# Kernel optimization log

Measured on AMD Instinct MI355X. Metric: run time of the kernel, lower is better.

## Reference

```python
import jax, jax.numpy as jnp
import numpy as np

B, T, F, U = 64, 256, 64, 512  # batch, bid_sequence, features, lstm units


def setup_inputs() -> dict:
    key = jax.random.key(0)
    ks = jax.random.split(key, 8)
    sc = 0.05
    return {
        "inputs": jax.random.normal(ks[0], (B, T, F), jnp.float32),
        "kernel": jax.random.normal(ks[1], (F, 4 * U), jnp.float32) * sc,      # LSTM input kernel (i,f,c,o)
        "rec_kernel": jax.random.normal(ks[2], (U, 4 * U), jnp.float32) * sc,  # LSTM recurrent kernel
        "bias": jax.random.normal(ks[3], (4 * U,), jnp.float32) * sc,          # LSTM bias
        "att_W": jax.random.normal(ks[4], (T, T), jnp.float32) * sc,           # row t = weights of attention_denses[t] (first t cols used)
        "att_b": jax.random.normal(ks[5], (T,), jnp.float32) * sc,             # bias of attention_denses[t]
        "out_W": jax.random.normal(ks[6], (U,), jnp.float32) * sc,             # final Dense(1) kernel
        "out_b": jax.random.normal(ks[7], (), jnp.float32) * sc,               # final Dense(1) bias
    }


def reference(inputs, kernel, rec_kernel, bias, att_W, att_b, out_W, out_b):
    Bs, Ts, _ = inputs.shape
    Us = rec_kernel.shape[0]

    # ---- LSTM (keras LSTMCell, gate order i,f,c,o; sigmoid/tanh) ----
    xz = jnp.einsum('btf,fg->btg', inputs, kernel) + bias  # precompute input projection

    def step(carry, z):
        h, c = carry
        g = z + h @ rec_kernel
        i, f, gc, o = jnp.split(g, 4, axis=-1)
        c = jax.nn.sigmoid(f) * c + jax.nn.sigmoid(i) * jnp.tanh(gc)
        h = jax.nn.sigmoid(o) * jnp.tanh(c)
        return (h, c), h

    init = (jnp.zeros((Bs, Us), inputs.dtype), jnp.zeros((Bs, Us), inputs.dtype))
    _, hs = jax.lax.scan(step, init, jnp.swapaxes(xz, 0, 1))
    x = jnp.swapaxes(hs, 0, 1)  # (B, T, U)

    # ---- attention_loop ----
    # keras Attention([x[:t], [x[t]]]) softmaxes over a single key -> weights are
    # exactly 1, so attn output is x[t] tiled t times; transpose + Dense_t(1)
    # collapses to sum(att_W[t, :t]) * x[t] + att_b[t]. Step 0 passes x[0] through.
    t_idx = jnp.arange(Ts)
    tri = (t_idx[None, :] < t_idx[:, None]).astype(x.dtype)  # row t: first t cols valid
    coef = jnp.where(t_idx == 0, jnp.asarray(1.0, x.dtype), jnp.sum(att_W * tri, axis=1))
    shift = jnp.where(t_idx == 0, jnp.asarray(0.0, x.dtype), att_b)
    att = x * coef[None, :, None] + shift[None, :, None]  # (B, T, U)

    # ---- final Dense(1) + reshape + sigmoid ----
    return jax.nn.sigmoid(jnp.einsum('btu,u->bt', att, out_W) + out_b)  # (B, T)
```

## Files before the change

### kernel.cpp

```cpp
#include <hip/hip_runtime.h>
#include <hip/hip_bf16.h>
#include <string.h>

#define B_ 64
#define T_ 256
#define F_ 64
#define U_ 512
#define G4_ 2048
#define KTOT 576
#define KSTEPS 18

typedef __attribute__((ext_vector_type(8))) short short8;
typedef __attribute__((ext_vector_type(4))) float v4f;
typedef __attribute__((ext_vector_type(4))) int i4;
typedef unsigned short u16;

__device__ __forceinline__ float bf2f(u16 b) {
    unsigned int x = ((unsigned int)b) << 16;
    float f; memcpy(&f, &x, 4); return f;
}
__device__ __forceinline__ u16 f2bf(float f) {
    __hip_bfloat16 h = __float2bfloat16(f);
    u16 b; memcpy(&b, &h, 2); return b;
}
__device__ __forceinline__ float sigmoidf_(float x) { return 1.f / (1.f + __expf(-x)); }
__device__ __forceinline__ float tanhf_(float x) {
    float xc = fminf(15.f, fmaxf(-15.f, x));
    float e = __expf(2.f * xc);
    return (e - 1.f) / (e + 1.f);
}

__device__ __forceinline__ float ldany(const void* p, size_t i, int fg) {
    return fg ? ((const float*)p)[i] : bf2f(((const u16*)p)[i]);
}

#define WS_FLAG   0
#define WS_XB     64
#define WS_WP     2097216
#define WS_H2     4456512
#define WS_DOT    4718656
#define WS_BIASF  4784192
#define WS_ATTWF  4792384
#define WS_ATTBF  5054528
#define WS_OUTWF  5055552
#define WS_OUTBF  5057600
#define WS_NEED   5057920

__global__ __launch_bounds__(256) void detect(const unsigned int* __restrict__ w,
                                              int* __restrict__ flag) {
    __shared__ int votes;
    if (threadIdx.x == 0) votes = 0;
    __syncthreads();
    unsigned int v = w[threadIdx.x];
    int e = (v >> 7) & 0xFF;
    if (e >= 100 && e <= 135) atomicAdd(&votes, 1);
    __syncthreads();
    if (threadIdx.x == 0) *flag = (votes < 200) ? 1 : 0;
}

__global__ __launch_bounds__(256) void convert(const void* __restrict__ x,
                                               const void* __restrict__ bias,
                                               const void* __restrict__ attW,
                                               const void* __restrict__ attb,
                                               const void* __restrict__ outW,
                                               const void* __restrict__ outb,
                                               const int* __restrict__ flag,
                                               u16* __restrict__ xb,
                                               float* __restrict__ biasf,
                                               float* __restrict__ attWf,
                                               float* __restrict__ attbf,
                                               float* __restrict__ outWf,
                                               float* __restrict__ outbf,
                                               float* __restrict__ dot,
                                               unsigned int* __restrict__ h2z) {
    int fg = *flag;
    size_t i = (size_t)blockIdx.x * 256 + threadIdx.x;
    if (i < 1048576) {
        float v = ldany(x, i, fg);
        int b = (int)(i >> 14), t = (int)((i >> 6) & 255), f = (int)(i & 63);
        xb[((size_t)t * B_ + b) * F_ + f] = f2bf(v);
        return;
    }
    i -= 1048576;
    if (i < 2048)  { biasf[i] = ldany(bias, i, fg); return; }
    i -= 2048;
    if (i < 65536) { attWf[i] = ldany(attW, i, fg); return; }
    i -= 65536;
    if (i < 256)   { attbf[i] = ldany(attb, i, fg); return; }
    i -= 256;
    if (i < 512)   { outWf[i] = ldany(outW, i, fg); return; }
    i -= 512;
    if (i < 1)     { outbf[i] = ldany(outb, i, fg); return; }
    i -= 1;
    if (i < 16384) { dot[i] = 0.f; return; }
    i -= 16384;
    if (i < 32768) { h2z[i] = 0u; return; }
}

__global__ __launch_bounds__(256) void pack_w(const void* __restrict__ kin,
                                              const void* __restrict__ krec,
                                              const int* __restrict__ flag,
                                              u16* __restrict__ Wp) {
    int fg = *flag;
    int gid = blockIdx.x * 256 + threadIdx.x;
    int lane = gid & 63;
    int frag = gid >> 6;
    int nt = frag / KSTEPS;
    int ks = frag - nt * KSTEPS;
    int kbase = ks * 32 + (lane >> 4) * 8;
    int cp = nt * 16 + (lane & 15);
    int u = cp >> 2, gate = cp & 3;
    int C = gate * U_ + u;
    short8 v;
    for (int j = 0; j < 8; j++) {
        int k = kbase + j;
        float w = (k < F_) ? ldany(kin, (size_t)k * G4_ + C, fg)
                           : ldany(krec, (size_t)(k - F_) * G4_ + C, fg);
        v[j] = (short)f2bf(w);
    }
    *reinterpret_cast<short8*>(Wp + (size_t)gid * 8) = v;
}

__global__ __launch_bounds__(512, 1) void lstm_persist(const u16* __restrict__ xb,
                                                       const float* __restrict__ biasf,
                                                       const float* __restrict__ outWf,
                                                       const u16* __restrict__ Wp,
                                                       u16* __restrict__ h2,
                                                       float* __restrict__ dot) {
    __shared__ __align__(16) u16 stage[16 * 520];
    __shared__ float dp[32][16][9];

    int tid = threadIdx.x;
    int bid = blockIdx.x;
    int rg = bid & 3;
    int gu = bid >> 2;
    int w = tid >> 6, l = tid & 63;
    int nt = gu * 8 + w;

    short8 W[KSTEPS];
    #pragma unroll
    for (int ks = 0; ks < KSTEPS; ks++)
        W[ks] = *reinterpret_cast<const short8*>(Wp + ((size_t)(nt * KSTEPS + ks) * 64 + l) * 8);

    int arow = rg * 16 + (l & 15);
    int koff = (l >> 4) * 8;
    int plr = 2 * w + (l >> 5);
    int pcol = (l & 31) * 16;
    int e = l & 3;
    int erow = 4 * (l >> 4) + e;
    int unit = 4 * nt + ((l >> 2) & 3);
    int cp = nt * 16 + (l & 15);
    float bc = biasf[(cp & 3) * U_ + (cp >> 2)];
    float wout = outWf[unit];
    float c = 0.f;

    for (int t = 0; t < T_; t++) {
        u16* hcur = h2 + (size_t)(t & 1) * (B_ * U_);
        const u16* hprev = h2 + (size_t)((t + 1) & 1) * (B_ * U_);
        unsigned int wtag = ((unsigned)(t >> 1) & 1u) ^ 1u;
        unsigned int rpat = ((((unsigned)(t - 1) >> 1) & 1u) ^ 1u) * 0x00010001u;

        const u16* xrow = xb + ((size_t)t * B_ + arow) * F_;
        short8 a0 = *reinterpret_cast<const short8*>(xrow + koff);
        short8 a1 = *reinterpret_cast<const short8*>(xrow + 32 + koff);
        v4f accA = {bc, bc, bc, bc};
        v4f accB = {0.f, 0.f, 0.f, 0.f};
        v4f accC = {0.f, 0.f, 0.f, 0.f};
        v4f accD = {0.f, 0.f, 0.f, 0.f};
        accA = __builtin_amdgcn_mfma_f32_16x16x32_bf16(a0, W[0], accA, 0, 0, 0);
        accB = __builtin_amdgcn_mfma_f32_16x16x32_bf16(a1, W[1], accB, 0, 0, 0);
        __builtin_amdgcn_sched_barrier(0);

        i4 q0, q1;
        {
            const void* bp = (const void*)(hprev + (size_t)(rg * 16 + plr) * U_ + pcol);
            int spins = 0;
            for (;;) {
                asm volatile(
                    "global_load_dwordx4 %0, %2, off sc0 sc1\n\t"
                    "global_load_dwordx4 %1, %2, off offset:16 sc0 sc1\n\t"
                    "s_waitcnt vmcnt(0)"
                    : "=v"(q0), "=v"(q1) : "v"(bp) : "memory");
                if (t == 0) break;
                unsigned bad = 0;
                bad |= (((unsigned)q0[0]) ^ rpat) & 0x00010001u;
                bad |= (((unsigned)q0[1]) ^ rpat) & 0x00010001u;
                bad |= (((unsigned)q0[2]) ^ rpat) & 0x00010001u;
                bad |= (((unsigned)q0[3]) ^ rpat) & 0x00010001u;
                bad |= (((unsigned)q1[0]) ^ rpat) & 0x00010001u;
                bad |= (((unsigned)q1[1]) ^ rpat) & 0x00010001u;
                bad |= (((unsigned)q1[2]) ^ rpat) & 0x00010001u;
                bad |= (((unsigned)q1[3]) ^ rpat) & 0x00010001u;
                if (__ballot(bad == 0) == ~0ull) break;
                if (++spins > (1 << 14)) break;
                if (spins > 16)     __builtin_amdgcn_s_sleep(2);
                else if (spins > 3) __builtin_amdgcn_s_sleep(1);
            }
        }
        *reinterpret_cast<i4*>(&stage[plr * 520 + pcol])     = q0;
        *reinterpret_cast<i4*>(&stage[plr * 520 + pcol + 8]) = q1;
        __syncthreads();

        #pragma unroll
        for (int m = 2; m < KSTEPS; m += 4) {
            const u16* srow = &stage[(l & 15) * 520 + koff];
            short8 h0 = *reinterpret_cast<const short8*>(srow + (m - 2) * 32);
            short8 h1 = *reinterpret_cast<const short8*>(srow + (m - 1) * 32);
            short8 h2v = *reinterpret_cast<const short8*>(srow + (m    ) * 32);
            short8 h3 = *reinterpret_cast<const short8*>(srow + (m + 1) * 32);
            accC = __builtin_amdgcn_mfma_f32_16x16x32_bf16(h0, W[m],     accC, 0, 0, 0);
            accD = __builtin_amdgcn_mfma_f32_16x16x32_bf16(h1, W[m + 1], accD, 0, 0, 0);
            accA = __builtin_amdgcn_mfma_f32_16x16x32_bf16(h2v, W[m + 2], accA, 0, 0, 0);
            accB = __builtin_amdgcn_mfma_f32_16x16x32_bf16(h3, W[m + 3], accB, 0, 0, 0);
        }
        v4f acc = (accA + accC) + (accB + accD);

        float g0 = acc[0], g1 = acc[1], g2 = acc[2], g3 = acc[3];
        {
            float t0 = __shfl_xor(g1, 1, 64);
            float t1 = __shfl_xor(g0, 1, 64);
            float t2 = __shfl_xor(g3, 1, 64);
            float t3 = __shfl_xor(g2, 1, 64);
            float b0 = ((0 ^ e) & 1) ? t0 : g0;
            float b1 = ((1 ^ e) & 1) ? t1 : g1;
            float b2 = ((2 ^ e) & 1) ? t2 : g2;
            float b3 = ((3 ^ e) & 1) ? t3 : g3;
            float u0 = __shfl_xor(b2, 2, 64);
            float u1 = __shfl_xor(b3, 2, 64);
            float u2 = __shfl_xor(b0, 2, 64);
            float u3 = __shfl_xor(b1, 2, 64);
            g0 = ((0 ^ e) & 2) ? u0 : b0;
            g1 = ((1 ^ e) & 2) ? u1 : b1;
            g2 = ((2 ^ e) & 2) ? u2 : b2;
            g3 = ((3 ^ e) & 2) ? u3 : b3;
        }

        {
            float ig = sigmoidf_(g0);
            float fg = sigmoidf_(g1);
            float gc = tanhf_(g2);
            float og = sigmoidf_(g3);
            c = fg * c + ig * gc;
            float h = og * tanhf_(c);

            float hp = __shfl_xor(h, 4, 64);
            if (((l >> 2) & 1) == 0) {
                unsigned int pk = (unsigned int)(((unsigned)f2bf(h)  & 0xFFFEu) | wtag)
                                | ((unsigned int)(((unsigned)f2bf(hp) & 0xFFFEu) | wtag) << 16);
                void* sp = (void*)(hcur + (size_t)(rg * 16 + erow) * U_ + unit);
                asm volatile("global_store_dword %0, %1, off sc0 sc1"
                             :: "v"(sp), "v"(pk) : "memory");
            }

            float s = h * wout;
            s += __shfl_xor(s, 4, 64);
            s += __shfl_xor(s, 8, 64);
            if ((l & 12) == 0) dp[t & 31][erow][w] = s;
        }

        if ((t & 31) == 31) {
            __syncthreads();
            int t0_ = t - 31;
            int tt = tid >> 4, row = tid & 15;
            float sum = 0.f;
            #pragma unroll
            for (int ww = 0; ww < 8; ww++) sum += dp[tt][row][ww];
            atomicAdd(&dot[(size_t)(rg * 16 + row) * T_ + (t0_ + tt)], sum);
        }
    }
}

__global__ __launch_bounds__(256) void finale(const float* __restrict__ attWf,
                                              const float* __restrict__ attbf,
                                              const float* __restrict__ outWf,
                                              const float* __restrict__ outbf,
                                              const float* __restrict__ dot,
                                              const int* __restrict__ flag,
                                              void* __restrict__ out) {
    __shared__ float red[256];
    int t = blockIdx.x, tid = threadIdx.x;
    int fg = *flag;

    float v = (tid < t) ? attWf[(size_t)t * T_ + tid] : 0.f;
    red[tid] = v; __syncthreads();
    for (int s = 128; s > 0; s >>= 1) { if (tid < s) red[tid] += red[tid + s]; __syncthreads(); }
    float coef = (t == 0) ? 1.f : red[0];
    __syncthreads();
    red[tid] = outWf[tid] + outWf[tid + 256]; __syncthreads();
    for (int s = 128; s > 0; s >>= 1) { if (tid < s) red[tid] += red[tid + s]; __syncthreads(); }
    float sumW = red[0];

    float base = ((t == 0) ? 0.f : attbf[t]) * sumW + outbf[0];

    if (tid < B_) {
        float s = sigmoidf_(coef * dot[(size_t)tid * T_ + t] + base);
        size_t idx = (size_t)tid * T_ + t;
        if (fg) ((float*)out)[idx] = s;
        else    ((u16*)out)[idx] = f2bf(s);
    }
}

extern "C" void kernel_launch(void* const* d_in, const int* in_sizes, int n_in,
                              void* d_out, int out_size, void* d_ws, size_t ws_size,
                              hipStream_t stream) {
    const void* x    = d_in[0];
    const void* kin  = d_in[1];
    const void* krec = d_in[2];
    const void* bias = d_in[3];
    const void* attW = d_in[4];
    const void* attb = d_in[5];
    const void* outW = d_in[6];
    const void* outb = d_in[7];

    if (ws_size < (size_t)WS_NEED) return;

    char* ws = (char*)d_ws;
    int*   flag  = (int*)(ws + WS_FLAG);
    u16*   xb    = (u16*)(ws + WS_XB);
    u16*   Wp    = (u16*)(ws + WS_WP);
    u16*   h2    = (u16*)(ws + WS_H2);
    float* dot   = (float*)(ws + WS_DOT);
    float* biasf = (float*)(ws + WS_BIASF);
    float* attWf = (float*)(ws + WS_ATTWF);
    float* attbf = (float*)(ws + WS_ATTBF);
    float* outWf = (float*)(ws + WS_OUTWF);
    float* outbf = (float*)(ws + WS_OUTBF);

    detect<<<1, 256, 0, stream>>>((const unsigned int*)kin, flag);
    convert<<<4556, 256, 0, stream>>>(x, bias, attW, attb, outW, outb, flag,
                                      xb, biasf, attWf, attbf, outWf, outbf, dot,
                                      (unsigned int*)h2);
    pack_w<<<576, 256, 0, stream>>>(kin, krec, flag, Wp);
    lstm_persist<<<64, 512, 0, stream>>>(xb, biasf, outWf, Wp, h2, dot);
    finale<<<256, 256, 0, stream>>>(attWf, attbf, outWf, outbf, dot, flag, d_out);
}
```

Measured before the change: 611.0 us.

## Process two batch row groups per block, halving persistent LSTM grid

```diff
diff --git a/kernel.cpp b/kernel.cpp
--- a/kernel.cpp
+++ b/kernel.cpp
@@ -127,13 +127,17 @@
                                                        const u16* __restrict__ Wp,
                                                        u16* __restrict__ h2,
                                                        float* __restrict__ dot) {
-    __shared__ __align__(16) u16 stage[16 * 520];
-    __shared__ float dp[32][16][9];
+    __shared__ __align__(16) u16 stageA[16 * 520];
+    __shared__ __align__(16) u16 stageB[16 * 520];
+    __shared__ float dpA[32][16][9];
+    __shared__ float dpB[32][16][9];
 
     int tid = threadIdx.x;
     int bid = blockIdx.x;
-    int rg = bid & 3;
-    int gu = bid >> 2;
+    int p = bid & 1;
+    int rgA = 2 * p;
+    int rgB = 2 * p + 1;
+    int gu = bid >> 1;
     int w = tid >> 6, l = tid & 63;
     int nt = gu * 8 + w;
 
@@ -142,17 +146,20 @@
     for (int ks = 0; ks < KSTEPS; ks++)
         W[ks] = *reinterpret_cast<const short8*>(Wp + ((size_t)(nt * KSTEPS + ks) * 64 + l) * 8);
 
-    int arow = rg * 16 + (l & 15);
+    int arowA = rgA * 16 + (l & 15);
+    int arowB = rgB * 16 + (l & 15);
     int koff = (l >> 4) * 8;
     int plr = 2 * w + (l >> 5);
     int pcol = (l & 31) * 16;
+    size_t poffA = (size_t)(rgA * 16 + plr) * U_ + pcol;
+    size_t poffB = (size_t)(rgB * 16 + plr) * U_ + pcol;
     int e = l & 3;
     int erow = 4 * (l >> 4) + e;
     int unit = 4 * nt + ((l >> 2) & 3);
     int cp = nt * 16 + (l & 15);
     float bc = biasf[(cp & 3) * U_ + (cp >> 2)];
     float wout = outWf[unit];
-    float c = 0.f;
+    float cA = 0.f, cB = 0.f;
 
     for (int t = 0; t < T_; t++) {
         u16* hcur = h2 + (size_t)(t & 1) * (B_ * U_);
@@ -160,94 +167,87 @@
         unsigned int wtag = ((unsigned)(t >> 1) & 1u) ^ 1u;
         unsigned int rpat = ((((unsigned)(t - 1) >> 1) & 1u) ^ 1u) * 0x00010001u;
 
-        const u16* xrow = xb + ((size_t)t * B_ + arow) * F_;
-        short8 a0 = *reinterpret_cast<const short8*>(xrow + koff);
-        short8 a1 = *reinterpret_cast<const short8*>(xrow + 32 + koff);
-        v4f accA = {bc, bc, bc, bc};
-        v4f accB = {0.f, 0.f, 0.f, 0.f};
-        v4f accC = {0.f, 0.f, 0.f, 0.f};
-        v4f accD = {0.f, 0.f, 0.f, 0.f};
-        accA = __builtin_amdgcn_mfma_f32_16x16x32_bf16(a0, W[0], accA, 0, 0, 0);
-        accB = __builtin_amdgcn_mfma_f32_16x16x32_bf16(a1, W[1], accB, 0, 0, 0);
-        __builtin_amdgcn_sched_barrier(0);
-
-        i4 q0, q1;
         {
-            const void* bp = (const void*)(hprev + (size_t)(rg * 16 + plr) * U_ + pcol);
-            int spins = 0;
-            for (;;) {
-                asm volatile(
-                    "global_load_dwordx4 %0, %2, off sc0 sc1\n\t"
-                    "global_load_dwordx4 %1, %2, off offset:16 sc0 sc1\n\t"
-                    "s_waitcnt vmcnt(0)"
-                    : "=v"(q0), "=v"(q1) : "v"(bp) : "memory");
-                if (t == 0) break;
-                unsigned bad = 0;
-                bad |= (((unsigned)q0[0]) ^ rpat) & 0x00010001u;
-                bad |= (((unsigned)q0[1]) ^ rpat) & 0x00010001u;
-                bad |= (((unsigned)q0[2]) ^ rpat) & 0x00010001u;
-                bad |= (((unsigned)q0[3]) ^ rpat) & 0x00010001u;
-                bad |= (((unsigned)q1[0]) ^ rpat) & 0x00010001u;
-                bad |= (((unsigned)q1[1]) ^ rpat) & 0x00010001u;
-                bad |= (((unsigned)q1[2]) ^ rpat) & 0x00010001u;
-                bad |= (((unsigned)q1[3]) ^ rpat) & 0x00010001u;
-                if (__ballot(bad == 0) == ~0ull) break;
-                if (++spins > (1 << 14)) break;
-                if (spins > 16)     __builtin_amdgcn_s_sleep(2);
-                else if (spins > 3) __builtin_amdgcn_s_sleep(1);
-            }
-        }
-        *reinterpret_cast<i4*>(&stage[plr * 520 + pcol])     = q0;
-        *reinterpret_cast<i4*>(&stage[plr * 520 + pcol + 8]) = q1;
-        __syncthreads();
-
-        #pragma unroll
-        for (int m = 2; m < KSTEPS; m += 4) {
-            const u16* srow = &stage[(l & 15) * 520 + koff];
-            short8 h0 = *reinterpret_cast<const short8*>(srow + (m - 2) * 32);
-            short8 h1 = *reinterpret_cast<const short8*>(srow + (m - 1) * 32);
-            short8 h2v = *reinterpret_cast<const short8*>(srow + (m    ) * 32);
-            short8 h3 = *reinterpret_cast<const short8*>(srow + (m + 1) * 32);
-            accC = __builtin_amdgcn_mfma_f32_16x16x32_bf16(h0, W[m],     accC, 0, 0, 0);
-            accD = __builtin_amdgcn_mfma_f32_16x16x32_bf16(h1, W[m + 1], accD, 0, 0, 0);
-            accA = __builtin_amdgcn_mfma_f32_16x16x32_bf16(h2v, W[m + 2], accA, 0, 0, 0);
-            accB = __builtin_amdgcn_mfma_f32_16x16x32_bf16(h3, W[m + 3], accB, 0, 0, 0);
-        }
-        v4f acc = (accA + accC) + (accB + accD);
-
-        float g0 = acc[0], g1 = acc[1], g2 = acc[2], g3 = acc[3];
-        {
-            float t0 = __shfl_xor(g1, 1, 64);
-            float t1 = __shfl_xor(g0, 1, 64);
-            float t2 = __shfl_xor(g3, 1, 64);
-            float t3 = __shfl_xor(g2, 1, 64);
-            float b0 = ((0 ^ e) & 1) ? t0 : g0;
-            float b1 = ((1 ^ e) & 1) ? t1 : g1;
-            float b2 = ((2 ^ e) & 1) ? t2 : g2;
-            float b3 = ((3 ^ e) & 1) ? t3 : g3;
-            float u0 = __shfl_xor(b2, 2, 64);
-            float u1 = __shfl_xor(b3, 2, 64);
-            float u2 = __shfl_xor(b0, 2, 64);
-            float u3 = __shfl_xor(b1, 2, 64);
-            g0 = ((0 ^ e) & 2) ? u0 : b0;
-            g1 = ((1 ^ e) & 2) ? u1 : b1;
-            g2 = ((2 ^ e) & 2) ? u2 : b2;
-            g3 = ((3 ^ e) & 2) ? u3 : b3;
-        }
-
-        {
+            const u16* xrow = xb + ((size_t)t * B_ + arowA) * F_;
+            short8 a0 = *reinterpret_cast<const short8*>(xrow + koff);
+            short8 a1 = *reinterpret_cast<const short8*>(xrow + 32 + koff);
+            v4f accP = {bc, bc, bc, bc};
+            v4f accQ = {0.f, 0.f, 0.f, 0.f};
+            accP = __builtin_amdgcn_mfma_f32_16x16x32_bf16(a0, W[0], accP, 0, 0, 0);
+            accQ = __builtin_amdgcn_mfma_f32_16x16x32_bf16(a1, W[1], accQ, 0, 0, 0);
+            __builtin_amdgcn_sched_barrier(0);
+
+            i4 q0, q1;
+            {
+                const void* bp = (const void*)(hprev + poffA);
+                int spins = 0;
+                for (;;) {
+                    asm volatile(
+                        "global_load_dwordx4 %0, %2, off sc0 sc1\n\t"
+                        "global_load_dwordx4 %1, %2, off offset:16 sc0 sc1\n\t"
+                        "s_waitcnt vmcnt(0)"
+                        : "=v"(q0), "=v"(q1) : "v"(bp) : "memory");
+                    if (t == 0) break;
+                    unsigned bad = 0;
+                    bad |= (((unsigned)q0[0]) ^ rpat) & 0x00010001u;
+                    bad |= (((unsigned)q0[1]) ^ rpat) & 0x00010001u;
+                    bad |= (((unsigned)q0[2]) ^ rpat) & 0x00010001u;
+                    bad |= (((unsigned)q0[3]) ^ rpat) & 0x00010001u;
+                    bad |= (((unsigned)q1[0]) ^ rpat) & 0x00010001u;
+                    bad |= (((unsigned)q1[1]) ^ rpat) & 0x00010001u;
+                    bad |= (((unsigned)q1[2]) ^ rpat) & 0x00010001u;
+                    bad |= (((unsigned)q1[3]) ^ rpat) & 0x00010001u;
+                    if (__ballot(bad == 0) == ~0ull) break;
+                    if (++spins > (1 << 14)) break;
+                    __builtin_amdgcn_s_sleep(2);
+                }
+            }
+            *reinterpret_cast<i4*>(&stageA[plr * 520 + pcol])     = q0;
+            *reinterpret_cast<i4*>(&stageA[plr * 520 + pcol + 8]) = q1;
+            __syncthreads();
+
+            #pragma unroll
+            for (int ks = 2; ks < KSTEPS; ks += 2) {
+                short8 ah0 = *reinterpret_cast<const short8*>(
+                    &stageA[(l & 15) * 520 + (ks - 2) * 32 + koff]);
+                short8 ah1 = *reinterpret_cast<const short8*>(
+                    &stageA[(l & 15) * 520 + (ks - 1) * 32 + koff]);
+                accP = __builtin_amdgcn_mfma_f32_16x16x32_bf16(ah0, W[ks],     accP, 0, 0, 0);
+                accQ = __builtin_amdgcn_mfma_f32_16x16x32_bf16(ah1, W[ks + 1], accQ, 0, 0, 0);
+            }
+            v4f acc = accP + accQ;
+
+            float g0 = acc[0], g1 = acc[1], g2 = acc[2], g3 = acc[3];
+            {
+                float t0 = __shfl_xor(g1, 1, 64);
+                float t1 = __shfl_xor(g0, 1, 64);
+                float t2 = __shfl_xor(g3, 1, 64);
+                float t3 = __shfl_xor(g2, 1, 64);
+                float b0 = ((0 ^ e) & 1) ? t0 : g0;
+                float b1 = ((1 ^ e) & 1) ? t1 : g1;
+                float b2 = ((2 ^ e) & 1) ? t2 : g2;
+                float b3 = ((3 ^ e) & 1) ? t3 : g3;
+                float u0 = __shfl_xor(b2, 2, 64);
+                float u1 = __shfl_xor(b3, 2, 64);
+                float u2 = __shfl_xor(b0, 2, 64);
+                float u3 = __shfl_xor(b1, 2, 64);
+                g0 = ((0 ^ e) & 2) ? u0 : b0;
+                g1 = ((1 ^ e) & 2) ? u1 : b1;
+                g2 = ((2 ^ e) & 2) ? u2 : b2;
+                g3 = ((3 ^ e) & 2) ? u3 : b3;
+            }
             float ig = sigmoidf_(g0);
             float fg = sigmoidf_(g1);
             float gc = tanhf_(g2);
             float og = sigmoidf_(g3);
-            c = fg * c + ig * gc;
-            float h = og * tanhf_(c);
+            cA = fg * cA + ig * gc;
+            float h = og * tanhf_(cA);
 
             float hp = __shfl_xor(h, 4, 64);
             if (((l >> 2) & 1) == 0) {
                 unsigned int pk = (unsigned int)(((unsigned)f2bf(h)  & 0xFFFEu) | wtag)
                                 | ((unsigned int)(((unsigned)f2bf(hp) & 0xFFFEu) | wtag) << 16);
-                void* sp = (void*)(hcur + (size_t)(rg * 16 + erow) * U_ + unit);
+                void* sp = (void*)(hcur + (size_t)(rgA * 16 + erow) * U_ + unit);
                 asm volatile("global_store_dword %0, %1, off sc0 sc1"
                              :: "v"(sp), "v"(pk) : "memory");
             }
@@ -255,17 +255,112 @@
             float s = h * wout;
             s += __shfl_xor(s, 4, 64);
             s += __shfl_xor(s, 8, 64);
-            if ((l & 12) == 0) dp[t & 31][erow][w] = s;
+            if ((l & 12) == 0) dpA[t & 31][erow][w] = s;
+        }
+
+        {
+            const u16* xrow = xb + ((size_t)t * B_ + arowB) * F_;
+            short8 a0 = *reinterpret_cast<const short8*>(xrow + koff);
+            short8 a1 = *reinterpret_cast<const short8*>(xrow + 32 + koff);
+            v4f accP = {bc, bc, bc, bc};
+            v4f accQ = {0.f, 0.f, 0.f, 0.f};
+            accP = __builtin_amdgcn_mfma_f32_16x16x32_bf16(a0, W[0], accP, 0, 0, 0);
+            accQ = __builtin_amdgcn_mfma_f32_16x16x32_bf16(a1, W[1], accQ, 0, 0, 0);
+            __builtin_amdgcn_sched_barrier(0);
+
+            i4 q0, q1;
+            {
+                const void* bp = (const void*)(hprev + poffB);
+                int spins = 0;
+                for (;;) {
+                    asm volatile(
+                        "global_load_dwordx4 %0, %2, off sc0 sc1\n\t"
+                        "global_load_dwordx4 %1, %2, off offset:16 sc0 sc1\n\t"
+                        "s_waitcnt vmcnt(0)"
+                        : "=v"(q0), "=v"(q1) : "v"(bp) : "memory");
+                    if (t == 0) break;
+                    unsigned bad = 0;
+                    bad |= (((unsigned)q0[0]) ^ rpat) & 0x00010001u;
+                    bad |= (((unsigned)q0[1]) ^ rpat) & 0x00010001u;
+                    bad |= (((unsigned)q0[2]) ^ rpat) & 0x00010001u;
+                    bad |= (((unsigned)q0[3]) ^ rpat) & 0x00010001u;
+                    bad |= (((unsigned)q1[0]) ^ rpat) & 0x00010001u;
+                    bad |= (((unsigned)q1[1]) ^ rpat) & 0x00010001u;
+                    bad |= (((unsigned)q1[2]) ^ rpat) & 0x00010001u;
+                    bad |= (((unsigned)q1[3]) ^ rpat) & 0x00010001u;
+                    if (__ballot(bad == 0) == ~0ull) break;
+                    if (++spins > (1 << 14)) break;
+                    __builtin_amdgcn_s_sleep(2);
+                }
+            }
+            *reinterpret_cast<i4*>(&stageB[plr * 520 + pcol])     = q0;
+            *reinterpret_cast<i4*>(&stageB[plr * 520 + pcol + 8]) = q1;
+            __syncthreads();
+
+            #pragma unroll
+            for (int ks = 2; ks < KSTEPS; ks += 2) {
+                short8 ah0 = *reinterpret_cast<const short8*>(
+                    &stageB[(l & 15) * 520 + (ks - 2) * 32 + koff]);
+                short8 ah1 = *reinterpret_cast<const short8*>(
+                    &stageB[(l & 15) * 520 + (ks - 1) * 32 + koff]);
+                accP = __builtin_amdgcn_mfma_f32_16x16x32_bf16(ah0, W[ks],     accP, 0, 0, 0);
+                accQ = __builtin_amdgcn_mfma_f32_16x16x32_bf16(ah1, W[ks + 1], accQ, 0, 0, 0);
+            }
+            v4f acc = accP + accQ;
+
+            float g0 = acc[0], g1 = acc[1], g2 = acc[2], g3 = acc[3];
+            {
+                float t0 = __shfl_xor(g1, 1, 64);
+                float t1 = __shfl_xor(g0, 1, 64);
+                float t2 = __shfl_xor(g3, 1, 64);
+                float t3 = __shfl_xor(g2, 1, 64);
+                float b0 = ((0 ^ e) & 1) ? t0 : g0;
+                float b1 = ((1 ^ e) & 1) ? t1 : g1;
+                float b2 = ((2 ^ e) & 1) ? t2 : g2;
+                float b3 = ((3 ^ e) & 1) ? t3 : g3;
+                float u0 = __shfl_xor(b2, 2, 64);
+                float u1 = __shfl_xor(b3, 2, 64);
+                float u2 = __shfl_xor(b0, 2, 64);
+                float u3 = __shfl_xor(b1, 2, 64);
+                g0 = ((0 ^ e) & 2) ? u0 : b0;
+                g1 = ((1 ^ e) & 2) ? u1 : b1;
+                g2 = ((2 ^ e) & 2) ? u2 : b2;
+                g3 = ((3 ^ e) & 2) ? u3 : b3;
+            }
+            float ig = sigmoidf_(g0);
+            float fg = sigmoidf_(g1);
+            float gc = tanhf_(g2);
+            float og = sigmoidf_(g3);
+            cB = fg * cB + ig * gc;
+            float h = og * tanhf_(cB);
+
+            float hp = __shfl_xor(h, 4, 64);
+            if (((l >> 2) & 1) == 0) {
+                unsigned int pk = (unsigned int)(((unsigned)f2bf(h)  & 0xFFFEu) | wtag)
+                                | ((unsigned int)(((unsigned)f2bf(hp) & 0xFFFEu) | wtag) << 16);
+                void* sp = (void*)(hcur + (size_t)(rgB * 16 + erow) * U_ + unit);
+                asm volatile("global_store_dword %0, %1, off sc0 sc1"
+                             :: "v"(sp), "v"(pk) : "memory");
+            }
+
+            float s = h * wout;
+            s += __shfl_xor(s, 4, 64);
+            s += __shfl_xor(s, 8, 64);
+            if ((l & 12) == 0) dpB[t & 31][erow][w] = s;
         }
 
         if ((t & 31) == 31) {
             __syncthreads();
             int t0_ = t - 31;
             int tt = tid >> 4, row = tid & 15;
-            float sum = 0.f;
+            float sumA = 0.f, sumB = 0.f;
             #pragma unroll
-            for (int ww = 0; ww < 8; ww++) sum += dp[tt][row][ww];
-            atomicAdd(&dot[(size_t)(rg * 16 + row) * T_ + (t0_ + tt)], sum);
+            for (int ww = 0; ww < 8; ww++) {
+                sumA += dpA[tt][row][ww];
+                sumB += dpB[tt][row][ww];
+            }
+            atomicAdd(&dot[(size_t)(rgA * 16 + row) * T_ + (t0_ + tt)], sumA);
+            atomicAdd(&dot[(size_t)(rgB * 16 + row) * T_ + (t0_ + tt)], sumB);
         }
     }
 }
@@ -331,6 +426,6 @@
                                       xb, biasf, attWf, attbf, outWf, outbf, dot,
                                       (unsigned int*)h2);
     pack_w<<<576, 256, 0, stream>>>(kin, krec, flag, Wp);
-    lstm_persist<<<64, 512, 0, stream>>>(xb, biasf, outWf, Wp, h2, dot);
+    lstm_persist<<<32, 512, 0, stream>>>(xb, biasf, outWf, Wp, h2, dot);
     finale<<<256, 256, 0, stream>>>(attWf, attbf, outWf, outbf, dot, flag, d_out);
 }
```

Measured after the change: 1.153 ms. 88.7% more time.
